# Optimization experiments

Hardware: AMD Instinct MI355X
Metric: run time of the kernel (lower is better)

The kernel has to match this reference:

```python
import jax, jax.numpy as jnp
import numpy as np

S, B, D, H, L = 1000, 4, 1024, 16, 4
HD = D // H
FF = 4 * D
V = 64
OUT = 64


def setup_inputs() -> dict:
    key = jax.random.key(0)
    ks = jax.random.split(key, 10)
    w = lambda k, shape: jax.random.normal(k, shape, jnp.float32) * 0.02
    return {
        'tokens': jax.random.randint(ks[0], (S, B), 0, V),
        'embed': w(ks[1], (V, D)),
        'Wq': w(ks[2], (L, D, D)), 'bq': jnp.zeros((L, D), jnp.float32),
        'Wk': w(ks[3], (L, D, D)), 'bk': jnp.zeros((L, D), jnp.float32),
        'Wv': w(ks[4], (L, D, D)), 'bv': jnp.zeros((L, D), jnp.float32),
        'Wo': w(ks[5], (L, D, D)), 'bo': jnp.zeros((L, D), jnp.float32),
        'ln1_g': jnp.ones((L, D), jnp.float32), 'ln1_b': jnp.zeros((L, D), jnp.float32),
        'ln2_g': jnp.ones((L, D), jnp.float32), 'ln2_b': jnp.zeros((L, D), jnp.float32),
        'W1': w(ks[6], (L, FF, D)), 'b1': jnp.zeros((L, FF), jnp.float32),
        'W2': w(ks[7], (L, D, FF)), 'b2': jnp.zeros((L, D), jnp.float32),
        'Wout': w(ks[8], (OUT, D)), 'bout': jnp.zeros((OUT,), jnp.float32),
    }


def _ln(x, g, b):
    m = x.mean(-1, keepdims=True)
    v = ((x - m) ** 2).mean(-1, keepdims=True)
    return (x - m) * jax.lax.rsqrt(v + 1e-5) * g + b


def _rope(x):
    # x: [B, H, S, HD]; matches RotaryEmbedding: x*cos + rotate_half(x)*sin
    hd = x.shape[-1]
    inv_freq = 1.0 / (10000.0 ** (jnp.arange(0, hd, 2, dtype=jnp.float32) / hd))
    t = jnp.arange(x.shape[2], dtype=jnp.float32)
    freqs = t[:, None] * inv_freq[None, :]          # [S, HD/2]
    emb = jnp.concatenate([freqs, freqs], -1)       # [S, HD]
    cos, sin = jnp.cos(emb), jnp.sin(emb)
    x1, x2 = jnp.split(x, 2, -1)
    rot = jnp.concatenate([-x2, x1], -1)
    return x * cos + rot * sin


def _attn(x, Wq, bq, Wk, bk, Wv, bv, Wo, bo):
    # x: [S, B, D]; manual rotary MHA path (eval: no dropout, masks None)
    s, b, d = x.shape
    scale = HD ** -0.5
    q = (jnp.einsum('sbd,ed->sbe', x, Wq) + bq) * scale
    k = jnp.einsum('sbd,ed->sbe', x, Wk) + bk
    v = jnp.einsum('sbd,ed->sbe', x, Wv) + bv
    split = lambda t: t.reshape(s, b, H, HD).transpose(1, 2, 0, 3)  # [B,H,S,HD]
    q, k, v = split(q), split(k), split(v)
    q, k = _rope(q), _rope(k)
    scores = jnp.einsum('bhsd,bhtd->bhst', q, k)
    p = jax.nn.softmax(scores, axis=-1)
    o = jnp.einsum('bhst,bhtd->bhsd', p, v)
    o = o.transpose(2, 0, 1, 3).reshape(s, b, d)
    return jnp.einsum('sbd,ed->sbe', o, Wo) + bo


def reference(tokens, embed, Wq, bq, Wk, bk, Wv, bv, Wo, bo,
              ln1_g, ln1_b, ln2_g, ln2_b, W1, b1, W2, b2, Wout, bout):
    x = embed[tokens]  # [S, B, D]
    for i in range(L):
        h = _ln(x, ln1_g[i], ln1_b[i])
        x = x + _attn(h, Wq[i], bq[i], Wk[i], bk[i], Wv[i], bv[i], Wo[i], bo[i])
        h = _ln(x, ln2_g[i], ln2_b[i])
        h = jax.nn.gelu(jnp.einsum('sbd,fd->sbf', h, W1[i]) + b1[i], approximate=False)
        x = x + jnp.einsum('sbf,df->sbd', h, W2[i]) + b2[i]
    return jnp.einsum('sbd,od->sbo', x, Wout) + bout
```

## Files before the change

kernel.cpp:

```cpp
#include <hip/hip_runtime.h>
#include <hip/hip_bf16.h>
#include <math.h>

#define S_   1000
#define B_   4
#define D_   1024
#define H_   16
#define HD_  64
#define L_   4
#define FF_  4096
#define N_   (S_*B_)

typedef __bf16 bf16x8 __attribute__((ext_vector_type(8)));
typedef float  f32x4  __attribute__((ext_vector_type(4)));
typedef __attribute__((address_space(3))) unsigned short lds_u16;

__device__ __forceinline__ unsigned short f2b(float f) {
    unsigned u = __builtin_bit_cast(unsigned, f);
    u = (u + 0x7FFFu + ((u >> 16) & 1u)) >> 16;
    return (unsigned short)u;
}
__device__ __forceinline__ float b2f(unsigned short s) {
    unsigned u = (unsigned)s << 16;
    return __builtin_bit_cast(float, u);
}

__device__ __forceinline__ void gl16(const void* g, void* l) {
    __builtin_amdgcn_global_load_lds(
        (const __attribute__((address_space(1))) unsigned int*)g,
        (__attribute__((address_space(3))) unsigned int*)l, 16, 0, 0);
}

__device__ __forceinline__ bf16x8 ldsr(unsigned addr) {
    bf16x8 r;
    asm volatile("ds_read_b128 %0, %1" : "=v"(r) : "v"(addr));
    return r;
}

__global__ void embed_kernel(const int* __restrict__ tokens,
                             const float* __restrict__ emb,
                             float* __restrict__ x) {
    int n = blockIdx.x;
    int tok = tokens[n];
    const float4* src = (const float4*)(emb + (size_t)tok * D_);
    float4* dst = (float4*)(x + (size_t)n * D_);
    dst[threadIdx.x] = src[threadIdx.x];
}

__global__ __launch_bounds__(256)
void cvtw_kernel(const float* __restrict__ wq, const float* __restrict__ wk,
                 const float* __restrict__ wv, const float* __restrict__ wo,
                 const float* __restrict__ w1, const float* __restrict__ w2,
                 unsigned short* __restrict__ dst) {
    const size_t M1 = (size_t)D_ * D_;
    const size_t M4 = (size_t)FF_ * D_;
    size_t i = ((size_t)blockIdx.x * 256 + threadIdx.x) * 4;
    const float* src; size_t off;
    if      (i < M1)        { src = wq; off = i; }
    else if (i < 2*M1)      { src = wk; off = i - M1; }
    else if (i < 3*M1)      { src = wv; off = i - 2*M1; }
    else if (i < 4*M1)      { src = wo; off = i - 3*M1; }
    else if (i < 4*M1+M4)   { src = w1; off = i - 4*M1; }
    else                    { src = w2; off = i - 4*M1 - M4; }
    float4 v = *(const float4*)(src + off);
    ushort4 u;
    u.x = f2b(v.x); u.y = f2b(v.y); u.z = f2b(v.z); u.w = f2b(v.w);
    *(ushort4*)(dst + i) = u;
}

__global__ __launch_bounds__(256)
void ln_kernel(const float* __restrict__ in,
               const float* __restrict__ g,
               const float* __restrict__ b,
               unsigned short* __restrict__ out) {
    int n = blockIdx.x;
    int tid = threadIdx.x;
    const float4* row = (const float4*)(in + (size_t)n * D_);
    float4 v = row[tid];
    float s  = v.x + v.y + v.z + v.w;
    float sq = v.x*v.x + v.y*v.y + v.z*v.z + v.w*v.w;
    #pragma unroll
    for (int off = 32; off; off >>= 1) {
        s  += __shfl_down(s, off);
        sq += __shfl_down(sq, off);
    }
    __shared__ float rs[4], rq[4];
    int wid = tid >> 6;
    if ((tid & 63) == 0) { rs[wid] = s; rq[wid] = sq; }
    __syncthreads();
    s  = rs[0] + rs[1] + rs[2] + rs[3];
    sq = rq[0] + rq[1] + rq[2] + rq[3];
    float mean = s * (1.0f / D_);
    float var  = sq * (1.0f / D_) - mean * mean;
    float rstd = rsqrtf(var + 1e-5f);
    float4 gg = ((const float4*)g)[tid];
    float4 bb = ((const float4*)b)[tid];
    ushort4 o;
    o.x = f2b((v.x - mean) * rstd * gg.x + bb.x);
    o.y = f2b((v.y - mean) * rstd * gg.y + bb.y);
    o.z = f2b((v.z - mean) * rstd * gg.z + bb.z);
    o.w = f2b((v.w - mean) * rstd * gg.w + bb.w);
    ((ushort4*)(out + (size_t)n * D_))[tid] = o;
}

template<int MODE>
__global__ __launch_bounds__(256, 2)
void agemm_kernel(const unsigned short* __restrict__ A,
                  const unsigned short* __restrict__ W,
                  const float* __restrict__ bb0, const float* __restrict__ bb1,
                  const float* __restrict__ bb2,
                  unsigned short* __restrict__ o0, unsigned short* __restrict__ o1,
                  unsigned short* __restrict__ o2,
                  int M, int K) {
    __shared__ __align__(16) unsigned short As[2][128 * 64];
    __shared__ __align__(16) unsigned short Bs[2][128 * 64];
    int tid = threadIdx.x;
    int w = tid >> 6, lane = tid & 63;
    int wr = w >> 1, wc = w & 1;
    int m0 = blockIdx.x * 128, e0 = blockIdx.y * 128;
    int l15 = lane & 15, l4 = lane >> 4, l7 = lane & 7;

    f32x4 acc[4][4] = {};

    auto stage = [&](int buf, int kt) {
        #pragma unroll
        for (int rep = 0; rep < 4; ++rep) {
            int slot = rep * 256 + tid;
            int r = slot >> 3, c = slot & 7;
            int ar = m0 + r; if (ar > M - 1) ar = M - 1;
            gl16(A + (size_t)ar * K + kt + (c ^ (r & 7)) * 8, &As[buf][slot * 8]);
        }
        #pragma unroll
        for (int rep = 0; rep < 4; ++rep) {
            int slot = rep * 256 + tid;
            int r = slot >> 3, c = slot & 7;
            gl16(W + (size_t)(e0 + r) * K + kt + (c ^ (r & 7)) * 8, &Bs[buf][slot * 8]);
        }
    };

    int aoff[4], boff[4];
    #pragma unroll
    for (int i = 0; i < 4; ++i) {
        aoff[i] = (wr * 64 + i * 16 + l15) * 128;
        boff[i] = (wc * 64 + i * 16 + l15) * 128;
    }

    stage(0, 0);
    asm volatile("s_waitcnt vmcnt(0)" ::: "memory");
    __builtin_amdgcn_sched_barrier(0);
    __builtin_amdgcn_s_barrier();

    int nk = K >> 6;
    for (int t = 0; t < nk; ++t) {
        int cur = t & 1;
        if (t + 1 < nk) stage(cur ^ 1, (t + 1) << 6);
        __builtin_amdgcn_sched_barrier(0);
        unsigned aB = (unsigned)(size_t)(lds_u16*)&As[cur][0];
        unsigned bB = (unsigned)(size_t)(lds_u16*)&Bs[cur][0];
        #pragma unroll
        for (int ks = 0; ks < 2; ++ks) {
            unsigned soff = (unsigned)((((ks * 4) + l4) ^ l7) * 16);
            bf16x8 av[4], bv[4];
            #pragma unroll
            for (int i = 0; i < 4; ++i) av[i] = ldsr(aB + aoff[i] + soff);
            #pragma unroll
            for (int j = 0; j < 4; ++j) bv[j] = ldsr(bB + boff[j] + soff);
            asm volatile("s_waitcnt lgkmcnt(0)" ::: "memory");
            __builtin_amdgcn_sched_barrier(0);
            __builtin_amdgcn_s_setprio(1);
            #pragma unroll
            for (int i = 0; i < 4; ++i)
                #pragma unroll
                for (int j = 0; j < 4; ++j)
                    acc[i][j] = __builtin_amdgcn_mfma_f32_16x16x32_bf16(av[i], bv[j], acc[i][j], 0, 0, 0);
            __builtin_amdgcn_s_setprio(0);
        }
        asm volatile("s_waitcnt vmcnt(0)" ::: "memory");
        __builtin_amdgcn_sched_barrier(0);
        __builtin_amdgcn_s_barrier();
    }

    if (MODE == 0) {
        int sel = e0 >> 10;
        int eobase = (e0 & 1023) + wc * 64;
        const float* bp = (sel == 0) ? bb0 : (sel == 1) ? bb1 : bb2;
        unsigned short* op = (sel == 0) ? o0 : (sel == 1) ? o1 : o2;
        float scale = (sel == 0) ? 0.125f : 1.0f;
        #pragma unroll
        for (int i = 0; i < 4; ++i) {
            int mrow = m0 + wr*64 + i*16 + l4*4;
            #pragma unroll
            for (int j = 0; j < 4; ++j) {
                int eo = eobase + j*16 + l15;
                float bval = bp[eo];
                #pragma unroll
                for (int r = 0; r < 4; ++r) {
                    int m = mrow + r;
                    if (m >= M) continue;
                    op[(size_t)m * 1024 + eo] = f2b((acc[i][j][r] + bval) * scale);
                }
            }
        }
    } else {
        #pragma unroll
        for (int i = 0; i < 4; ++i) {
            int mrow = m0 + wr*64 + i*16 + l4*4;
            #pragma unroll
            for (int j = 0; j < 4; ++j) {
                int e = e0 + wc*64 + j*16 + l15;
                float bval = bb0[e];
                #pragma unroll
                for (int r = 0; r < 4; ++r) {
                    int m = mrow + r;
                    if (m >= M) continue;
                    float val = acc[i][j][r] + bval;
                    val = 0.5f * val * (1.0f + erff(val * 0.70710678118654752f));
                    o0[(size_t)m * FF_ + e] = f2b(val);
                }
            }
        }
    }
}

__global__ __launch_bounds__(256, 2)
void dgemm_kernel(const unsigned short* __restrict__ A,
                  const unsigned short* __restrict__ W,
                  const float* __restrict__ bias,
                  const float* __restrict__ res,
                  float* __restrict__ out,
                  int M, int K) {
    __shared__ __align__(16) unsigned short As[2][128 * 64];
    __shared__ __align__(16) unsigned short Bs[2][64 * 64];
    int tid = threadIdx.x;
    int w = tid >> 6, lane = tid & 63;
    int wr = w >> 1, wc = w & 1;
    int m0 = blockIdx.x * 128, e0 = blockIdx.y * 64;
    int l15 = lane & 15, l4 = lane >> 4, l7 = lane & 7;

    f32x4 acc[4][2] = {};

    auto stage = [&](int buf, int kt) {
        #pragma unroll
        for (int rep = 0; rep < 4; ++rep) {
            int slot = rep * 256 + tid;
            int r = slot >> 3, c = slot & 7;
            int ar = m0 + r; if (ar > M - 1) ar = M - 1;
            gl16(A + (size_t)ar * K + kt + (c ^ (r & 7)) * 8, &As[buf][slot * 8]);
        }
        #pragma unroll
        for (int rep = 0; rep < 2; ++rep) {
            int slot = rep * 256 + tid;
            int r = slot >> 3, c = slot & 7;
            gl16(W + (size_t)(e0 + r) * K + kt + (c ^ (r & 7)) * 8, &Bs[buf][slot * 8]);
        }
    };

    int aoff[4], boff[2];
    #pragma unroll
    for (int i = 0; i < 4; ++i) aoff[i] = (wr * 64 + i * 16 + l15) * 128;
    #pragma unroll
    for (int j = 0; j < 2; ++j) boff[j] = (wc * 32 + j * 16 + l15) * 128;

    stage(0, 0);
    asm volatile("s_waitcnt vmcnt(0)" ::: "memory");
    __builtin_amdgcn_sched_barrier(0);
    __builtin_amdgcn_s_barrier();

    int nk = K >> 6;
    for (int t = 0; t < nk; ++t) {
        int cur = t & 1;
        if (t + 1 < nk) stage(cur ^ 1, (t + 1) << 6);
        __builtin_amdgcn_sched_barrier(0);
        unsigned aB = (unsigned)(size_t)(lds_u16*)&As[cur][0];
        unsigned bB = (unsigned)(size_t)(lds_u16*)&Bs[cur][0];
        #pragma unroll
        for (int ks = 0; ks < 2; ++ks) {
            unsigned soff = (unsigned)((((ks * 4) + l4) ^ l7) * 16);
            bf16x8 av[4], bv[2];
            #pragma unroll
            for (int i = 0; i < 4; ++i) av[i] = ldsr(aB + aoff[i] + soff);
            #pragma unroll
            for (int j = 0; j < 2; ++j) bv[j] = ldsr(bB + boff[j] + soff);
            asm volatile("s_waitcnt lgkmcnt(0)" ::: "memory");
            __builtin_amdgcn_sched_barrier(0);
            __builtin_amdgcn_s_setprio(1);
            #pragma unroll
            for (int i = 0; i < 4; ++i)
                #pragma unroll
                for (int j = 0; j < 2; ++j)
                    acc[i][j] = __builtin_amdgcn_mfma_f32_16x16x32_bf16(av[i], bv[j], acc[i][j], 0, 0, 0);
            __builtin_amdgcn_s_setprio(0);
        }
        asm volatile("s_waitcnt vmcnt(0)" ::: "memory");
        __builtin_amdgcn_sched_barrier(0);
        __builtin_amdgcn_s_barrier();
    }

    #pragma unroll
    for (int i = 0; i < 4; ++i) {
        int mrow = m0 + wr*64 + i*16 + l4*4;
        #pragma unroll
        for (int j = 0; j < 2; ++j) {
            int e = e0 + wc*32 + j*16 + l15;
            float bval = bias[e];
            #pragma unroll
            for (int r = 0; r < 4; ++r) {
                int m = mrow + r;
                if (m >= M) continue;
                out[(size_t)m * 1024 + e] = acc[i][j][r] + bval + res[(size_t)m * 1024 + e];
            }
        }
    }
}

__global__ __launch_bounds__(256)
void gemm_kernel(const float* __restrict__ A, const float* __restrict__ W,
                 const float* __restrict__ bias, float* __restrict__ C,
                 int M, int K, int E) {
    __shared__ float As[32][64];
    __shared__ float Ws[32][64];
    int tid = threadIdx.x;
    int m0 = blockIdx.x * 64, e0 = blockIdx.y * 64;
    int tx = tid & 15, ty = tid >> 4;
    int lrow = tid >> 2;
    int lkc  = (tid & 3) * 8;
    float acc[4][4] = {};
    const float* Arow = A + (size_t)(m0 + lrow) * K + lkc;
    const float* Wrow = W + (size_t)(e0 + lrow) * K + lkc;
    bool aval = (m0 + lrow) < M;

    for (int k0 = 0; k0 < K; k0 += 32) {
        float4 a0 = make_float4(0.f,0.f,0.f,0.f), a1 = a0;
        if (aval) {
            a0 = *(const float4*)(Arow + k0);
            a1 = *(const float4*)(Arow + k0 + 4);
        }
        float4 w0 = *(const float4*)(Wrow + k0);
        float4 w1 = *(const float4*)(Wrow + k0 + 4);
        As[lkc+0][lrow] = a0.x; As[lkc+1][lrow] = a0.y;
        As[lkc+2][lrow] = a0.z; As[lkc+3][lrow] = a0.w;
        As[lkc+4][lrow] = a1.x; As[lkc+5][lrow] = a1.y;
        As[lkc+6][lrow] = a1.z; As[lkc+7][lrow] = a1.w;
        Ws[lkc+0][lrow] = w0.x; Ws[lkc+1][lrow] = w0.y;
        Ws[lkc+2][lrow] = w0.z; Ws[lkc+3][lrow] = w0.w;
        Ws[lkc+4][lrow] = w1.x; Ws[lkc+5][lrow] = w1.y;
        Ws[lkc+6][lrow] = w1.z; Ws[lkc+7][lrow] = w1.w;
        __syncthreads();
        #pragma unroll
        for (int kk = 0; kk < 32; ++kk) {
            float4 a = *(const float4*)(&As[kk][ty*4]);
            float4 ww = *(const float4*)(&Ws[kk][tx*4]);
            acc[0][0] += a.x*ww.x; acc[0][1] += a.x*ww.y; acc[0][2] += a.x*ww.z; acc[0][3] += a.x*ww.w;
            acc[1][0] += a.y*ww.x; acc[1][1] += a.y*ww.y; acc[1][2] += a.y*ww.z; acc[1][3] += a.y*ww.w;
            acc[2][0] += a.z*ww.x; acc[2][1] += a.z*ww.y; acc[2][2] += a.z*ww.z; acc[2][3] += a.z*ww.w;
            acc[3][0] += a.w*ww.x; acc[3][1] += a.w*ww.y; acc[3][2] += a.w*ww.z; acc[3][3] += a.w*ww.w;
        }
        __syncthreads();
    }
    #pragma unroll
    for (int i = 0; i < 4; ++i) {
        int m = m0 + ty*4 + i;
        if (m >= M) continue;
        #pragma unroll
        for (int j = 0; j < 4; ++j) {
            int e = e0 + tx*4 + j;
            C[(size_t)m * E + e] = acc[i][j] + bias[e];
        }
    }
}

__global__ void ropeb_kernel(unsigned short* __restrict__ x) {
    int idx = blockIdx.x * 256 + threadIdx.x;
    if (idx >= N_ * H_ * 32) return;
    int j = idx & 31;
    int h = (idx >> 5) & (H_ - 1);
    int n = idx >> 9;
    int s = n >> 2;
    float inv = __expf(-(float)j * 0.2878231366242557f);
    float ang = (float)s * inv;
    float sn, cs;
    __sincosf(ang, &sn, &cs);
    unsigned short* p = x + (size_t)n * D_ + h * HD_ + j;
    float a = b2f(p[0]), c = b2f(p[32]);
    p[0]  = f2b(a * cs - c * sn);
    p[32] = f2b(c * cs + a * sn);
}

__global__ __launch_bounds__(256)
void vtr_kernel(const unsigned short* __restrict__ vin,
                unsigned short* __restrict__ vout) {
    __shared__ unsigned short T[64][65];
    int tt = blockIdx.x;
    int bh = blockIdx.y;
    int b = bh >> 4, h = bh & 15;
    int tid = threadIdx.x;
    #pragma unroll
    for (int rep = 0; rep < 2; ++rep) {
        int slot = rep * 256 + tid;
        int r = slot >> 3, ch = slot & 7;
        int t = tt * 64 + r;
        unsigned short e[8] = {0,0,0,0,0,0,0,0};
        if (t < S_) {
            const unsigned short* src = vin + ((size_t)t * B_ + b) * D_ + h * HD_ + ch * 8;
            *(ushort4*)&e[0] = *(const ushort4*)(src);
            *(ushort4*)&e[4] = *(const ushort4*)(src + 4);
        }
        #pragma unroll
        for (int u = 0; u < 8; ++u) T[r][ch*8+u] = e[u];
    }
    __syncthreads();
    #pragma unroll
    for (int rep = 0; rep < 2; ++rep) {
        int slot = rep * 256 + tid;
        int d = slot >> 3, ch = slot & 7;
        unsigned short e[8];
        #pragma unroll
        for (int u = 0; u < 8; ++u) e[u] = T[ch*8+u][d];
        unsigned short* dst = vout + ((size_t)bh * 64 + d) * 1024 + tt * 64 + ch * 8;
        *(ushort4*)(dst)     = *(ushort4*)&e[0];
        *(ushort4*)(dst + 4) = *(ushort4*)&e[4];
    }
}

__global__ __launch_bounds__(256)
void mattn_kernel(const unsigned short* __restrict__ qg,
                  const unsigned short* __restrict__ kg,
                  const unsigned short* __restrict__ vt,
                  unsigned short* __restrict__ o) {
    __shared__ __align__(16) unsigned short Ks[64 * 64];
    __shared__ __align__(16) unsigned short Vs[64 * 64];
    __shared__ __align__(16) unsigned short Ps[4][16 * 64];

    int bid = blockIdx.x;
    int qt = bid & 15;
    int bh = bid >> 4;
    int b = bh >> 4, h = bh & 15;
    int tid = threadIdx.x;
    int w = tid >> 6, lane = tid & 63;
    int l15 = lane & 15, l4 = lane >> 4, l7 = lane & 7;
    int q0 = qt * 64 + w * 16;

    int srow = lane >> 3;
    int schunk = ((lane & 7) ^ srow) * 8;

    bf16x8 qfr[2];
    {
        int qr = q0 + l15; if (qr > S_ - 1) qr = S_ - 1;
        const unsigned short* qrow = qg + ((size_t)qr * B_ + b) * D_ + h * HD_;
        qfr[0] = *(const bf16x8*)(qrow + l4 * 8);
        qfr[1] = *(const bf16x8*)(qrow + 32 + l4 * 8);
    }

    f32x4 accO[4] = {};
    float mreg[4] = {-1e30f, -1e30f, -1e30f, -1e30f};
    float lreg[4] = {0.f, 0.f, 0.f, 0.f};

    for (int t0 = 0; t0 < 1024; t0 += 64) {
        __syncthreads();
        #pragma unroll
        for (int c = 0; c < 2; ++c) {
            int r0 = w * 16 + c * 8;
            int tr = t0 + r0 + srow; if (tr > S_ - 1) tr = S_ - 1;
            gl16(kg + ((size_t)tr * B_ + b) * D_ + h * HD_ + schunk, &Ks[r0 * 64]);
            gl16(vt + ((size_t)bh * 64 + r0 + srow) * 1024 + t0 + schunk, &Vs[r0 * 64]);
        }
        __syncthreads();

        f32x4 s[4] = {};
        #pragma unroll
        for (int ks = 0; ks < 2; ++ks) {
            int cc = ks * 4 + l4;
            int slot = (cc ^ l7) * 16;
            #pragma unroll
            for (int j = 0; j < 4; ++j) {
                bf16x8 kf = *(const bf16x8*)((const char*)Ks + (j*16 + l15) * 128 + slot);
                s[j] = __builtin_amdgcn_mfma_f32_16x16x32_bf16(qfr[ks], kf, s[j], 0, 0, 0);
            }
        }
        #pragma unroll
        for (int j = 0; j < 4; ++j) {
            int t = t0 + j * 16 + l15;
            if (t >= S_) { s[j][0] = -1e30f; s[j][1] = -1e30f; s[j][2] = -1e30f; s[j][3] = -1e30f; }
        }
        float rm[4], sc[4], rsum[4];
        #pragma unroll
        for (int r = 0; r < 4; ++r)
            rm[r] = fmaxf(fmaxf(s[0][r], s[1][r]), fmaxf(s[2][r], s[3][r]));
        #pragma unroll
        for (int mk = 1; mk <= 8; mk <<= 1) {
            #pragma unroll
            for (int r = 0; r < 4; ++r) rm[r] = fmaxf(rm[r], __shfl_xor(rm[r], mk));
        }
        #pragma unroll
        for (int r = 0; r < 4; ++r) {
            float mn = fmaxf(mreg[r], rm[r]);
            sc[r] = __expf(mreg[r] - mn);
            mreg[r] = mn;
            rsum[r] = 0.f;
        }
        #pragma unroll
        for (int j = 0; j < 4; ++j) {
            int inb = (j * 16 + l15) * 2;
            #pragma unroll
            for (int r = 0; r < 4; ++r) {
                float p = __expf(s[j][r] - mreg[r]);
                rsum[r] += p;
                int row = l4 * 4 + r;
                *(unsigned short*)((char*)&Ps[w][0] + row * 128 +
                    ((((inb >> 4) ^ (row & 7)) << 4)) + (inb & 15)) = f2b(p);
            }
        }
        #pragma unroll
        for (int mk = 1; mk <= 8; mk <<= 1) {
            #pragma unroll
            for (int r = 0; r < 4; ++r) rsum[r] += __shfl_xor(rsum[r], mk);
        }
        #pragma unroll
        for (int r = 0; r < 4; ++r) lreg[r] = lreg[r] * sc[r] + rsum[r];
        #pragma unroll
        for (int j = 0; j < 4; ++j) {
            accO[j][0] *= sc[0]; accO[j][1] *= sc[1];
            accO[j][2] *= sc[2]; accO[j][3] *= sc[3];
        }
        #pragma unroll
        for (int ks = 0; ks < 2; ++ks) {
            int cc = ks * 4 + l4;
            int slot = (cc ^ l7) * 16;
            bf16x8 pf = *(const bf16x8*)((const char*)&Ps[w][0] + l15 * 128 + slot);
            #pragma unroll
            for (int j = 0; j < 4; ++j) {
                bf16x8 vf = *(const bf16x8*)((const char*)Vs + (j*16 + l15) * 128 + slot);
                accO[j] = __builtin_amdgcn_mfma_f32_16x16x32_bf16(pf, vf, accO[j], 0, 0, 0);
            }
        }
    }
    #pragma unroll
    for (int r = 0; r < 4; ++r) {
        int q = q0 + l4 * 4 + r;
        if (q >= S_) continue;
        float inv = 1.0f / lreg[r];
        unsigned short* orow = o + ((size_t)q * B_ + b) * D_ + h * HD_;
        #pragma unroll
        for (int j = 0; j < 4; ++j)
            orow[j * 16 + l15] = f2b(accO[j][r] * inv);
    }
}

extern "C" void kernel_launch(void* const* d_in, const int* in_sizes, int n_in,
                              void* d_out, int out_size, void* d_ws, size_t ws_size,
                              hipStream_t stream) {
    const int*   tokens = (const int*)  d_in[0];
    const float* Wemb   = (const float*)d_in[1];
    const float* Wq     = (const float*)d_in[2];
    const float* bq     = (const float*)d_in[3];
    const float* Wk     = (const float*)d_in[4];
    const float* bk     = (const float*)d_in[5];
    const float* Wv     = (const float*)d_in[6];
    const float* bv     = (const float*)d_in[7];
    const float* Wo     = (const float*)d_in[8];
    const float* bo     = (const float*)d_in[9];
    const float* ln1g   = (const float*)d_in[10];
    const float* ln1b   = (const float*)d_in[11];
    const float* ln2g   = (const float*)d_in[12];
    const float* ln2b   = (const float*)d_in[13];
    const float* W1     = (const float*)d_in[14];
    const float* b1     = (const float*)d_in[15];
    const float* W2     = (const float*)d_in[16];
    const float* b2     = (const float*)d_in[17];
    const float* Wout   = (const float*)d_in[18];
    const float* bout   = (const float*)d_in[19];
    float* out = (float*)d_out;

    const size_t ND = (size_t)N_ * D_;
    const size_t NF = (size_t)N_ * FF_;
    const size_t M1 = (size_t)D_ * D_;
    const size_t M4 = (size_t)FF_ * D_;
    const size_t VT = (size_t)64 * 64 * 1024;

    float* x  = (float*)d_ws;
    unsigned short* hb = (unsigned short*)(x + ND);
    unsigned short* qb = hb + ND;
    unsigned short* kb = qb + ND;
    unsigned short* vb = kb + ND;
    unsigned short* ob = vb + ND;
    unsigned short* vt = ob + ND;
    unsigned short* f1 = vt + VT;
    unsigned short* wb = f1 + NF;

    dim3 blk(256);
    embed_kernel<<<N_, blk, 0, stream>>>(tokens, Wemb, x);

    dim3 gQKV(32, 24);
    dim3 gW1(32, 32);
    dim3 gE64(32, 16);
    dim3 gCv(12288);
    int rth = N_ * H_ * 32;
    dim3 gR((rth + 255) / 256);
    dim3 gVt(16, 64);
    dim3 gAt(16 * 64);
    dim3 gOut((N_ + 63) / 64, 1);

    for (int l = 0; l < L_; ++l) {
        cvtw_kernel<<<gCv, blk, 0, stream>>>(Wq + l*M1, Wk + l*M1, Wv + l*M1,
                                             Wo + l*M1, W1 + l*M4, W2 + l*M4, wb);
        ln_kernel<<<N_, blk, 0, stream>>>(x, ln1g + l*D_, ln1b + l*D_, hb);
        agemm_kernel<0><<<gQKV, blk, 0, stream>>>(hb, wb,
            bq + l*D_, bk + l*D_, bv + l*D_, qb, kb, vb, N_, D_);
        ropeb_kernel<<<gR, blk, 0, stream>>>(qb);
        ropeb_kernel<<<gR, blk, 0, stream>>>(kb);
        vtr_kernel<<<gVt, blk, 0, stream>>>(vb, vt);
        mattn_kernel<<<gAt, blk, 0, stream>>>(qb, kb, vt, ob);
        dgemm_kernel<<<gE64, blk, 0, stream>>>(ob, wb + 3*M1,
            bo + l*D_, x, x, N_, D_);
        ln_kernel<<<N_, blk, 0, stream>>>(x, ln2g + l*D_, ln2b + l*D_, hb);
        agemm_kernel<1><<<gW1, blk, 0, stream>>>(hb, wb + 4*M1,
            b1 + l*FF_, nullptr, nullptr, f1, nullptr, nullptr, N_, D_);
        dgemm_kernel<<<gE64, blk, 0, stream>>>(f1, wb + 4*M1 + M4,
            b2 + l*D_, x, x, N_, FF_);
    }
    gemm_kernel<<<gOut, blk, 0, stream>>>(x, Wout, bout, out, N_, D_, 64);
}
```

Before: 1.189 ms.

## Fuse RoPE into QKV GEMM epilogue and shrink GEMM tile to 128x64

The QKV/W1 GEMM now uses 128x64 output tiles, so each block's N-range covers exactly one 64-wide head. That lets the QKV epilogue apply rotary embedding to Q and K in registers, pairing columns d and d+32. This removes the two separate RoPE kernel launches and their bf16 read-modify-write passes over Q and K. The smaller tile doubles the grid and lowers per-block data reuse, which adds load traffic per FLOP in both the QKV and W1 GEMMs. The RoPE is also now computed from fp32 accumulators before bf16 rounding rather than after.

Result: faster. 1.128 ms (-5.1%).

```diff
diff --git a/kernel.cpp b/kernel.cpp
--- a/kernel.cpp
+++ b/kernel.cpp
@@ -105,7 +105,7 @@
 
 template<int MODE>
 __global__ __launch_bounds__(256, 2)
-void agemm_kernel(const unsigned short* __restrict__ A,
+void egemm_kernel(const unsigned short* __restrict__ A,
                   const unsigned short* __restrict__ W,
                   const float* __restrict__ bb0, const float* __restrict__ bb1,
                   const float* __restrict__ bb2,
@@ -113,14 +113,13 @@
                   unsigned short* __restrict__ o2,
                   int M, int K) {
     __shared__ __align__(16) unsigned short As[2][128 * 64];
-    __shared__ __align__(16) unsigned short Bs[2][128 * 64];
+    __shared__ __align__(16) unsigned short Bs[2][64 * 64];
     int tid = threadIdx.x;
     int w = tid >> 6, lane = tid & 63;
-    int wr = w >> 1, wc = w & 1;
-    int m0 = blockIdx.x * 128, e0 = blockIdx.y * 128;
+    int m0 = blockIdx.x * 128, e0 = blockIdx.y * 64;
     int l15 = lane & 15, l4 = lane >> 4, l7 = lane & 7;
 
-    f32x4 acc[4][4] = {};
+    f32x4 acc[2][4] = {};
 
     auto stage = [&](int buf, int kt) {
         #pragma unroll
@@ -131,19 +130,18 @@
             gl16(A + (size_t)ar * K + kt + (c ^ (r & 7)) * 8, &As[buf][slot * 8]);
         }
         #pragma unroll
-        for (int rep = 0; rep < 4; ++rep) {
+        for (int rep = 0; rep < 2; ++rep) {
             int slot = rep * 256 + tid;
             int r = slot >> 3, c = slot & 7;
             gl16(W + (size_t)(e0 + r) * K + kt + (c ^ (r & 7)) * 8, &Bs[buf][slot * 8]);
         }
     };
 
-    int aoff[4], boff[4];
-    #pragma unroll
-    for (int i = 0; i < 4; ++i) {
-        aoff[i] = (wr * 64 + i * 16 + l15) * 128;
-        boff[i] = (wc * 64 + i * 16 + l15) * 128;
-    }
+    int aoff[2], boff[4];
+    #pragma unroll
+    for (int i = 0; i < 2; ++i) aoff[i] = (w * 32 + i * 16 + l15) * 128;
+    #pragma unroll
+    for (int j = 0; j < 4; ++j) boff[j] = (j * 16 + l15) * 128;
 
     stage(0, 0);
     asm volatile("s_waitcnt vmcnt(0)" ::: "memory");
@@ -160,16 +158,16 @@
         #pragma unroll
         for (int ks = 0; ks < 2; ++ks) {
             unsigned soff = (unsigned)((((ks * 4) + l4) ^ l7) * 16);
-            bf16x8 av[4], bv[4];
-            #pragma unroll
-            for (int i = 0; i < 4; ++i) av[i] = ldsr(aB + aoff[i] + soff);
+            bf16x8 av[2], bv[4];
+            #pragma unroll
+            for (int i = 0; i < 2; ++i) av[i] = ldsr(aB + aoff[i] + soff);
             #pragma unroll
             for (int j = 0; j < 4; ++j) bv[j] = ldsr(bB + boff[j] + soff);
             asm volatile("s_waitcnt lgkmcnt(0)" ::: "memory");
             __builtin_amdgcn_sched_barrier(0);
             __builtin_amdgcn_s_setprio(1);
             #pragma unroll
-            for (int i = 0; i < 4; ++i)
+            for (int i = 0; i < 2; ++i)
                 #pragma unroll
                 for (int j = 0; j < 4; ++j)
                     acc[i][j] = __builtin_amdgcn_mfma_f32_16x16x32_bf16(av[i], bv[j], acc[i][j], 0, 0, 0);
@@ -182,32 +180,60 @@
 
     if (MODE == 0) {
         int sel = e0 >> 10;
-        int eobase = (e0 & 1023) + wc * 64;
+        int eobase = e0 & 1023;
         const float* bp = (sel == 0) ? bb0 : (sel == 1) ? bb1 : bb2;
         unsigned short* op = (sel == 0) ? o0 : (sel == 1) ? o1 : o2;
-        float scale = (sel == 0) ? 0.125f : 1.0f;
-        #pragma unroll
-        for (int i = 0; i < 4; ++i) {
-            int mrow = m0 + wr*64 + i*16 + l4*4;
-            #pragma unroll
-            for (int j = 0; j < 4; ++j) {
-                int eo = eobase + j*16 + l15;
-                float bval = bp[eo];
+        if (sel == 2) {
+            #pragma unroll
+            for (int i = 0; i < 2; ++i) {
+                int mrow = m0 + w*32 + i*16 + l4*4;
                 #pragma unroll
-                for (int r = 0; r < 4; ++r) {
-                    int m = mrow + r;
-                    if (m >= M) continue;
-                    op[(size_t)m * 1024 + eo] = f2b((acc[i][j][r] + bval) * scale);
+                for (int j = 0; j < 4; ++j) {
+                    int eo = eobase + j*16 + l15;
+                    float bval = bp[eo];
+                    #pragma unroll
+                    for (int r = 0; r < 4; ++r) {
+                        int m = mrow + r;
+                        if (m >= M) continue;
+                        op[(size_t)m * 1024 + eo] = f2b(acc[i][j][r] + bval);
+                    }
                 }
             }
+        } else {
+            float scale = (sel == 0) ? 0.125f : 1.0f;
+            #pragma unroll
+            for (int i = 0; i < 2; ++i) {
+                int mrow = m0 + w*32 + i*16 + l4*4;
+                #pragma unroll
+                for (int jj = 0; jj < 2; ++jj) {
+                    int d5 = jj*16 + l15;
+                    int eo_a = eobase + d5;
+                    int eo_b = eo_a + 32;
+                    float ba = bp[eo_a], bbv = bp[eo_b];
+                    float invf = __expf(-(float)d5 * 0.2878231366242557f);
+                    #pragma unroll
+                    for (int r = 0; r < 4; ++r) {
+                        int m = mrow + r;
+                        if (m >= M) continue;
+                        int s = m >> 2;
+                        float ang = (float)s * invf;
+                        float sn, cs;
+                        __sincosf(ang, &sn, &cs);
+                        float a = acc[i][jj][r]   + ba;
+                        float c = acc[i][jj+2][r] + bbv;
+                        op[(size_t)m * 1024 + eo_a] = f2b((a*cs - c*sn) * scale);
+                        op[(size_t)m * 1024 + eo_b] = f2b((c*cs + a*sn) * scale);
+                    }
+                }
+            }
         }
     } else {
         #pragma unroll
-        for (int i = 0; i < 4; ++i) {
-            int mrow = m0 + wr*64 + i*16 + l4*4;
+        for (int i = 0; i < 2; ++i) {
+            int mrow = m0 + w*32 + i*16 + l4*4;
             #pragma unroll
             for (int j = 0; j < 4; ++j) {
-                int e = e0 + wc*64 + j*16 + l15;
+                int e = e0 + j*16 + l15;
                 float bval = bb0[e];
                 #pragma unroll
                 for (int r = 0; r < 4; ++r) {
@@ -367,23 +393,6 @@
             C[(size_t)m * E + e] = acc[i][j] + bias[e];
         }
     }
-}
-
-__global__ void ropeb_kernel(unsigned short* __restrict__ x) {
-    int idx = blockIdx.x * 256 + threadIdx.x;
-    if (idx >= N_ * H_ * 32) return;
-    int j = idx & 31;
-    int h = (idx >> 5) & (H_ - 1);
-    int n = idx >> 9;
-    int s = n >> 2;
-    float inv = __expf(-(float)j * 0.2878231366242557f);
-    float ang = (float)s * inv;
-    float sn, cs;
-    __sincosf(ang, &sn, &cs);
-    unsigned short* p = x + (size_t)n * D_ + h * HD_ + j;
-    float a = b2f(p[0]), c = b2f(p[32]);
-    p[0]  = f2b(a * cs - c * sn);
-    p[32] = f2b(c * cs + a * sn);
 }
 
 __global__ __launch_bounds__(256)
@@ -590,12 +599,10 @@
     dim3 blk(256);
     embed_kernel<<<N_, blk, 0, stream>>>(tokens, Wemb, x);
 
-    dim3 gQKV(32, 24);
-    dim3 gW1(32, 32);
+    dim3 gQKV(32, 48);
+    dim3 gW1(32, 64);
     dim3 gE64(32, 16);
     dim3 gCv(12288);
-    int rth = N_ * H_ * 32;
-    dim3 gR((rth + 255) / 256);
     dim3 gVt(16, 64);
     dim3 gAt(16 * 64);
     dim3 gOut((N_ + 63) / 64, 1);
@@ -604,16 +611,14 @@
         cvtw_kernel<<<gCv, blk, 0, stream>>>(Wq + l*M1, Wk + l*M1, Wv + l*M1,
                                              Wo + l*M1, W1 + l*M4, W2 + l*M4, wb);
         ln_kernel<<<N_, blk, 0, stream>>>(x, ln1g + l*D_, ln1b + l*D_, hb);
-        agemm_kernel<0><<<gQKV, blk, 0, stream>>>(hb, wb,
+        egemm_kernel<0><<<gQKV, blk, 0, stream>>>(hb, wb,
             bq + l*D_, bk + l*D_, bv + l*D_, qb, kb, vb, N_, D_);
-        ropeb_kernel<<<gR, blk, 0, stream>>>(qb);
-        ropeb_kernel<<<gR, blk, 0, stream>>>(kb);
         vtr_kernel<<<gVt, blk, 0, stream>>>(vb, vt);
         mattn_kernel<<<gAt, blk, 0, stream>>>(qb, kb, vt, ob);
         dgemm_kernel<<<gE64, blk, 0, stream>>>(ob, wb + 3*M1,
             bo + l*D_, x, x, N_, D_);
         ln_kernel<<<N_, blk, 0, stream>>>(x, ln2g + l*D_, ln2b + l*D_, hb);
-        agemm_kernel<1><<<gW1, blk, 0, stream>>>(hb, wb + 4*M1,
+        egemm_kernel<1><<<gW1, blk, 0, stream>>>(hb, wb + 4*M1,
             b1 + l*FF_, nullptr, nullptr, f1, nullptr, nullptr, N_, D_);
         dgemm_kernel<<<gE64, blk, 0, stream>>>(f1, wb + 4*M1 + M4,
             b2 + l*D_, x, x, N_, FF_);
```
